# Kernel optimization log

Measured on AMD Instinct MI355X. Metric: run time of the kernel, lower is better.

Reference implementation:

```python
import jax, jax.numpy as jnp
import numpy as np

N = 100000
E = 3200000
D_IN = 83
D_HID = 1024
N_CLASSES = 25


def setup_inputs() -> dict:
    key = jax.random.key(0)
    ks = jax.random.split(key, 10)
    feature = jax.random.normal(ks[0], (N, D_IN), dtype=jnp.float32)
    edge_row = jax.random.randint(ks[1], (E,), 0, N, dtype=jnp.int32)
    edge_col = jax.random.randint(ks[2], (E,), 0, N, dtype=jnp.int32)
    adj_val = jax.random.uniform(ks[3], (E,), dtype=jnp.float32)
    # Conv1d(1 -> 4, kernel 5, pad 2): weight [out=4, in=1, k=5]
    conv_w = jax.random.normal(ks[4], (4, 1, 5), dtype=jnp.float32) * 0.2
    conv_b = jnp.zeros((4,), dtype=jnp.float32)
    # GCN weights (kaiming-uniform-like scale), zero biases
    W1 = jax.random.uniform(ks[5], (D_IN, D_HID), dtype=jnp.float32,
                            minval=-1.0, maxval=1.0) * np.sqrt(6.0 / D_IN)
    b1 = jnp.zeros((D_HID,), dtype=jnp.float32)
    W2 = jax.random.uniform(ks[6], (D_HID, N_CLASSES), dtype=jnp.float32,
                            minval=-1.0, maxval=1.0) * np.sqrt(6.0 / D_HID)
    b2 = jnp.zeros((N_CLASSES,), dtype=jnp.float32)
    return {"feature": feature, "conv_w": conv_w, "conv_b": conv_b,
            "W1": W1, "b1": b1, "W2": W2, "b2": b2,
            "adj_val": adj_val, "edge_row": edge_row, "edge_col": edge_col}


def _spmm(vals, row, col, X):
    # sparse(adj) @ X : gather source rows, scale by edge value, scatter-add to dest
    return jax.ops.segment_sum(vals[:, None] * X[col], row, num_segments=N)


def reference(feature, conv_w, conv_b, W1, b1, W2, b2, adj_val, edge_row, edge_col):
    # Conv1d prelude: [N,1,83] -> [N,4,83], sum over channels, relu -> [N,83]
    x = jax.lax.conv_general_dilated(
        feature[:, None, :], conv_w, window_strides=(1,), padding=[(2, 2)],
        dimension_numbers=("NCH", "OIH", "NCH"))
    x = x + conv_b[None, :, None]
    x = jax.nn.relu(jnp.sum(x, axis=1))
    # GCN layer 1: relu(A @ (x W1) + b1)
    h = jax.nn.relu(_spmm(adj_val, edge_row, edge_col, x @ W1) + b1)
    # GCN layer 2: A @ (h W2) + b2
    logits = _spmm(adj_val, edge_row, edge_col, h @ W2) + b2
    return logits
```

## Files before the change

kernel.cpp:

```cpp
#include <hip/hip_runtime.h>

#define NN   100000
#define EE   3200000
#define DIN  83
#define DHID 1024
#define NCLS 25
#define XPAD 96
#define ZPAD 32

#define NBK     391
#define CHUNK   8192

typedef __attribute__((__ext_vector_type__(8))) short sh8;
typedef __attribute__((__ext_vector_type__(4))) float f4_t;

static __device__ __forceinline__ float relu_(float v) { return v > 0.f ? v : 0.f; }

static __device__ __forceinline__ unsigned short f2bf(float f) {
  unsigned int u = __float_as_uint(f);
  unsigned int r = u + 0x7FFFu + ((u >> 16) & 1u);
  return (unsigned short)(r >> 16);
}
static __device__ __forceinline__ float bflo(unsigned int q) {
  return __uint_as_float(q << 16);
}
static __device__ __forceinline__ float bfhi(unsigned int q) {
  return __uint_as_float(q & 0xFFFF0000u);
}

__global__ void conv_relu_k(const float* __restrict__ feature,
                            const float* __restrict__ conv_w,
                            const float* __restrict__ conv_b,
                            unsigned short* __restrict__ x) {
  float ws0 = conv_w[0] + conv_w[5] + conv_w[10] + conv_w[15];
  float ws1 = conv_w[1] + conv_w[6] + conv_w[11] + conv_w[16];
  float ws2 = conv_w[2] + conv_w[7] + conv_w[12] + conv_w[17];
  float ws3 = conv_w[3] + conv_w[8] + conv_w[13] + conv_w[18];
  float ws4 = conv_w[4] + conv_w[9] + conv_w[14] + conv_w[19];
  float bs  = conv_b[0] + conv_b[1] + conv_b[2] + conv_b[3];
  const int total = NN * XPAD;
  for (int idx = blockIdx.x * blockDim.x + threadIdx.x; idx < total;
       idx += gridDim.x * blockDim.x) {
    int n = idx / XPAD;
    int i = idx - n * XPAD;
    unsigned short o = 0;
    if (i < DIN) {
      const float* f = feature + (size_t)n * DIN;
      float acc = bs;
      if (i >= 2)      acc += ws0 * f[i - 2];
      if (i >= 1)      acc += ws1 * f[i - 1];
      acc += ws2 * f[i];
      if (i + 1 < DIN) acc += ws3 * f[i + 1];
      if (i + 2 < DIN) acc += ws4 * f[i + 2];
      o = f2bf(relu_(acc));
    }
    x[idx] = o;
  }
}

__global__ void zero_int_k(int* __restrict__ p, int total) {
  for (int i = blockIdx.x * blockDim.x + threadIdx.x; i < total;
       i += gridDim.x * blockDim.x)
    p[i] = 0;
}

__global__ void w1t_k(const float* __restrict__ W1, unsigned short* __restrict__ w1t) {
  int idx = blockIdx.x * blockDim.x + threadIdx.x;
  if (idx >= DHID * XPAD) return;
  int k = idx / DHID;
  int n = idx - k * DHID;
  float v = (k < DIN) ? W1[k * DHID + n] : 0.f;
  w1t[n * XPAD + k] = f2bf(v);
}

__global__ void w2t_k(const float* __restrict__ W2, unsigned short* __restrict__ w2t) {
  int idx = blockIdx.x * blockDim.x + threadIdx.x;
  if (idx >= 32 * DHID) return;
  int k = idx / 32;
  int n = idx - k * 32;
  float v = (n < NCLS) ? W2[k * NCLS + n] : 0.f;
  w2t[n * DHID + k] = f2bf(v);
}


__global__ __launch_bounds__(256) void bucket_hist_k(
    const int* __restrict__ row, int* __restrict__ gbk) {
  __shared__ int cnt[NBK];
  const int tid = threadIdx.x;
  for (int b = tid; b < NBK; b += 256) cnt[b] = 0;
  __syncthreads();
  const int cb = blockIdx.x * CHUNK;
  const int csize = (cb + CHUNK <= EE) ? CHUNK : (EE - cb);
  for (int i = tid; i < csize; i += 256)
    atomicAdd(&cnt[row[cb + i] >> 8], 1);
  __syncthreads();
  for (int b = tid; b < NBK; b += 256)
    if (cnt[b]) atomicAdd(&gbk[b * 16], cnt[b]);
}

__global__ void scan_buckets_k(const int* __restrict__ gbk,
                               int* __restrict__ bbase, int* __restrict__ gcur) {
  __shared__ int sd[512];
  int t = threadIdx.x;
  int v = (t < NBK) ? gbk[t * 16] : 0;
  sd[t] = v;
  __syncthreads();
  for (int off = 1; off < 512; off <<= 1) {
    int add = (t >= off) ? sd[t - off] : 0;
    __syncthreads();
    sd[t] += add;
    __syncthreads();
  }
  if (t < NBK) {
    int excl = sd[t] - v;
    bbase[t] = excl;
    gcur[t * 16] = excl;
  }
  if (t == 0) bbase[NBK] = EE;
}

__global__ __launch_bounds__(256) void partition_k(
    const float* __restrict__ vals, const int* __restrict__ row,
    const int* __restrict__ col, int* __restrict__ gcur,
    int2* __restrict__ tmp) {
  __shared__ int cnt[NBK];
  __shared__ int sc[512];
  __shared__ int es[NBK + 1];
  __shared__ int lcur[NBK];
  __shared__ int gbase[NBK];
  __shared__ int2 staged[CHUNK];
  const int tid = threadIdx.x;
  const int cb = blockIdx.x * CHUNK;
  const int csize = (cb + CHUNK <= EE) ? CHUNK : (EE - cb);

  for (int b = tid; b < NBK; b += 256) cnt[b] = 0;
  __syncthreads();
  for (int i = tid; i < csize; i += 256)
    atomicAdd(&cnt[row[cb + i] >> 8], 1);
  __syncthreads();
  sc[tid]       = (tid < NBK) ? cnt[tid] : 0;
  sc[tid + 256] = (tid + 256 < NBK) ? cnt[tid + 256] : 0;
  __syncthreads();
  for (int off = 1; off < 512; off <<= 1) {
    int a0 = (tid >= off) ? sc[tid - off] : 0;
    int a1 = (tid + 256 >= off) ? sc[tid + 256 - off] : 0;
    __syncthreads();
    sc[tid] += a0;
    sc[tid + 256] += a1;
    __syncthreads();
  }
  for (int b = tid; b < NBK; b += 256) {
    int e = sc[b] - cnt[b];
    es[b] = e;
    lcur[b] = e;
  }
  if (tid == 0) es[NBK] = csize;
  __syncthreads();
  for (int b = tid; b < NBK; b += 256)
    gbase[b] = cnt[b] ? atomicAdd(&gcur[b * 16], cnt[b]) : 0;
  __syncthreads();
  for (int i = tid; i < csize; i += 256) {
    int r = row[cb + i];
    int lpos = atomicAdd(&lcur[r >> 8], 1);
    staged[lpos] = make_int2(col[cb + i] | ((r & 255) << 17),
                             __float_as_int(vals[cb + i]));
  }
  __syncthreads();
  {
    const int w = tid >> 6;
    const int lane = tid & 63;
    for (int b = w; b < NBK; b += 4) {
      int st = es[b], en = es[b + 1];
      int gb = gbase[b];
      for (int j = st + lane; j < en; j += 64)
        tmp[gb + (j - st)] = staged[j];
    }
  }
}

__global__ __launch_bounds__(256) void fine_scatter2_k(
    const int* __restrict__ bbase, const int2* __restrict__ tmp,
    int2* __restrict__ csr, int* __restrict__ offs, int* __restrict__ counts) {
  __shared__ int cnt[256];
  __shared__ int sd[256];
  __shared__ int lcur[256];
  const int tid = threadIdx.x;
  const int b = blockIdx.x;
  const int r0 = b * 256;
  const int gstart = bbase[b];
  const int nedge = bbase[b + 1] - gstart;
  cnt[tid] = 0;
  __syncthreads();
  for (int i = tid; i < nedge; i += 256)
    atomicAdd(&cnt[((unsigned)tmp[gstart + i].x) >> 17], 1);
  __syncthreads();
  int v = cnt[tid];
  sd[tid] = v;
  __syncthreads();
  for (int off = 1; off < 256; off <<= 1) {
    int add = (tid >= off) ? sd[tid - off] : 0;
    __syncthreads();
    sd[tid] += add;
    __syncthreads();
  }
  int excl = gstart + sd[tid] - v;
  int r = r0 + tid;
  if (r < NN) {
    offs[r] = excl;
    counts[r] = v;
  }
  lcur[tid] = excl;
  __syncthreads();
  for (int i = tid; i < nedge; i += 256) {
    int2 p = tmp[gstart + i];
    int rl = ((unsigned)p.x) >> 17;
    int pos = atomicAdd(&lcur[rl], 1);
    csr[pos] = make_int2(p.x & 0x1FFFF, p.y);
  }
}

__global__ __launch_bounds__(256) void spmm83_g(
    const int* __restrict__ offs, const int* __restrict__ cnt,
    const int2* __restrict__ csr, const unsigned short* __restrict__ x,
    unsigned short* __restrict__ ax) {
  int wave = (int)((blockIdx.x * blockDim.x + threadIdx.x) >> 6);
  int lane = threadIdx.x & 63;
  if (wave >= NN) return;
  int s = offs[wave];
  int n = cnt[wave];
  const bool act = lane < 48;
  const int d2 = lane * 2;
  float a0 = 0.f, a1 = 0.f;
  int i = 0;
  for (; i + 8 <= n; i += 8) {
    int2 p[8];
#pragma unroll
    for (int u = 0; u < 8; ++u) p[u] = csr[s + i + u];
    if (act) {
      unsigned int q[8];
#pragma unroll
      for (int u = 0; u < 8; ++u)
        q[u] = *(const unsigned int*)&x[(size_t)p[u].x * XPAD + d2];
#pragma unroll
      for (int u = 0; u < 8; ++u) {
        float v = __int_as_float(p[u].y);
        a0 += v * bflo(q[u]);
        a1 += v * bfhi(q[u]);
      }
    }
  }
  for (; i < n; ++i) {
    int2 p = csr[s + i];
    if (act) {
      unsigned int q = *(const unsigned int*)&x[(size_t)p.x * XPAD + d2];
      float v = __int_as_float(p.y);
      a0 += v * bflo(q);
      a1 += v * bfhi(q);
    }
  }
  if (act) {
    unsigned int o = (unsigned int)f2bf(a0) | ((unsigned int)f2bf(a1) << 16);
    *(unsigned int*)&ax[(size_t)wave * XPAD + d2] = o;
  }
}

__global__ __launch_bounds__(256) void spmm25_g(
    const int* __restrict__ offs, const int* __restrict__ cnt,
    const int2* __restrict__ csr, const unsigned short* __restrict__ zb,
    const float* __restrict__ b2, float* __restrict__ out) {
  int gw = (int)((blockIdx.x * blockDim.x + threadIdx.x) >> 6);
  int lane = threadIdx.x & 63;
  int sub = lane >> 4;
  int d2 = (lane & 15) * 2;
  int r = gw * 4 + sub;
  if (r >= NN) return;
  int s = offs[r];
  int n = cnt[r];
  float a0 = 0.f, a1 = 0.f;
  int i = 0;
  for (; i + 4 <= n; i += 4) {
    int2 p0 = csr[s + i + 0];
    int2 p1 = csr[s + i + 1];
    int2 p2 = csr[s + i + 2];
    int2 p3 = csr[s + i + 3];
    unsigned int q0 = *(const unsigned int*)&zb[(size_t)p0.x * ZPAD + d2];
    unsigned int q1 = *(const unsigned int*)&zb[(size_t)p1.x * ZPAD + d2];
    unsigned int q2 = *(const unsigned int*)&zb[(size_t)p2.x * ZPAD + d2];
    unsigned int q3 = *(const unsigned int*)&zb[(size_t)p3.x * ZPAD + d2];
    float v0 = __int_as_float(p0.y), v1 = __int_as_float(p1.y);
    float v2 = __int_as_float(p2.y), v3 = __int_as_float(p3.y);
    a0 += v0 * bflo(q0) + v1 * bflo(q1) + v2 * bflo(q2) + v3 * bflo(q3);
    a1 += v0 * bfhi(q0) + v1 * bfhi(q1) + v2 * bfhi(q2) + v3 * bfhi(q3);
  }
  for (; i < n; ++i) {
    int2 p = csr[s + i];
    unsigned int q = *(const unsigned int*)&zb[(size_t)p.x * ZPAD + d2];
    float v = __int_as_float(p.y);
    a0 += v * bflo(q);
    a1 += v * bfhi(q);
  }
  if (d2 < NCLS)     out[(size_t)r * NCLS + d2]     = a0 + b2[d2];
  if (d2 + 1 < NCLS) out[(size_t)r * NCLS + d2 + 1] = a1 + b2[d2 + 1];
}

__global__ __launch_bounds__(256) void fused_mlp_mfma(
    const unsigned short* __restrict__ axg, const unsigned short* __restrict__ w1t,
    const float* __restrict__ b1, const unsigned short* __restrict__ w2t,
    unsigned short* __restrict__ zb) {
  __shared__ __align__(16) unsigned short axs[64 * 104];
  __shared__ __align__(16) unsigned short hs[64 * 264];
  __shared__ float b1s[DHID];
  const int tid = threadIdx.x;
  const int n0 = blockIdx.x * 64;

  for (int idx = tid; idx < 64 * 12; idx += 256) {
    int m = idx / 12;
    int c8 = idx - m * 12;
    int node = n0 + m;
    sh8 v = {0, 0, 0, 0, 0, 0, 0, 0};
    if (node < NN) v = *(const sh8*)&axg[(size_t)node * XPAD + c8 * 8];
    *(sh8*)&axs[m * 104 + c8 * 8] = v;
  }
  for (int i = tid; i < DHID; i += 256) b1s[i] = b1[i];
  __syncthreads();

  const int lane = tid & 63;
  const int w = tid >> 6;
  const int quad = lane >> 4;
  const int tn = lane & 15;
  const int m0 = w * 16;

  sh8 a1[4][3];
#pragma unroll
  for (int mt = 0; mt < 4; ++mt)
#pragma unroll
    for (int kc = 0; kc < 3; ++kc)
      a1[mt][kc] = *(const sh8*)&axs[(mt * 16 + tn) * 104 + kc * 32 + quad * 8];

  f4_t z0 = {0.f, 0.f, 0.f, 0.f}, z1 = {0.f, 0.f, 0.f, 0.f};

  for (int c = 0; c < 4; ++c) {
    const int cb = c * 256;
#pragma unroll
    for (int nti = 0; nti < 4; ++nti) {
      const int nt = w * 4 + nti;
      const int ng = cb + nt * 16 + tn;
      const unsigned short* wr = &w1t[(size_t)ng * XPAD + quad * 8];
      sh8 b0 = *(const sh8*)&wr[0];
      sh8 b1f = *(const sh8*)&wr[32];
      sh8 b2f = *(const sh8*)&wr[64];
      float bias = b1s[ng];
#pragma unroll
      for (int mt = 0; mt < 4; ++mt) {
        f4_t acc = {0.f, 0.f, 0.f, 0.f};
        acc = __builtin_amdgcn_mfma_f32_16x16x32_bf16(a1[mt][0], b0, acc, 0, 0, 0);
        acc = __builtin_amdgcn_mfma_f32_16x16x32_bf16(a1[mt][1], b1f, acc, 0, 0, 0);
        acc = __builtin_amdgcn_mfma_f32_16x16x32_bf16(a1[mt][2], b2f, acc, 0, 0, 0);
#pragma unroll
        for (int r = 0; r < 4; ++r) {
          float v = relu_(acc[r] + bias);
          hs[(mt * 16 + quad * 4 + r) * 264 + nt * 16 + tn] = f2bf(v);
        }
      }
    }
    __syncthreads();
#pragma unroll
    for (int kc = 0; kc < 8; ++kc) {
      sh8 a2 = *(const sh8*)&hs[(m0 + tn) * 264 + kc * 32 + quad * 8];
      sh8 bl = *(const sh8*)&w2t[(size_t)tn * DHID + cb + kc * 32 + quad * 8];
      z0 = __builtin_amdgcn_mfma_f32_16x16x32_bf16(a2, bl, z0, 0, 0, 0);
      sh8 bh = *(const sh8*)&w2t[(size_t)(16 + tn) * DHID + cb + kc * 32 + quad * 8];
      z1 = __builtin_amdgcn_mfma_f32_16x16x32_bf16(a2, bh, z1, 0, 0, 0);
    }
    __syncthreads();
  }

#pragma unroll
  for (int r = 0; r < 4; ++r) {
    int node = n0 + m0 + quad * 4 + r;
    if (node < NN) {
      zb[(size_t)node * ZPAD + tn]      = f2bf(z0[r]);
      zb[(size_t)node * ZPAD + 16 + tn] = f2bf(z1[r]);
    }
  }
}

extern "C" void kernel_launch(void* const* d_in, const int* in_sizes, int n_in,
                              void* d_out, int out_size, void* d_ws, size_t ws_size,
                              hipStream_t stream) {
  const float* feature = (const float*)d_in[0];
  const float* conv_w  = (const float*)d_in[1];
  const float* conv_b  = (const float*)d_in[2];
  const float* W1      = (const float*)d_in[3];
  const float* b1      = (const float*)d_in[4];
  const float* W2      = (const float*)d_in[5];
  const float* b2      = (const float*)d_in[6];
  const float* adj     = (const float*)d_in[7];
  const int*   erow    = (const int*)d_in[8];
  const int*   ecol    = (const int*)d_in[9];
  float* out = (float*)d_out;

  char* B = (char*)d_ws;
  size_t o = 0;
  auto alloc = [&](size_t bytes, size_t align) -> void* {
    o = (o + align - 1) & ~(align - 1);
    void* p = B + o;
    o += bytes;
    return p;
  };
  unsigned short* x    = (unsigned short*)alloc((size_t)NN * XPAD * 2, 16);
  unsigned short* ax   = (unsigned short*)alloc((size_t)NN * XPAD * 2, 16);
  unsigned short* zb   = (unsigned short*)alloc((size_t)NN * ZPAD * 2, 16);
  int*   counts  = (int*)alloc((size_t)NN * 4, 16);
  int*   offs    = (int*)alloc((size_t)NN * 4, 16);
  int*   gcur    = (int*)alloc((size_t)NBK * 16 * 4, 64);
  int*   gbk     = (int*)alloc((size_t)NBK * 16 * 4, 64);
  int*   bbase   = (int*)alloc((size_t)(NBK + 1) * 4, 16);
  unsigned short* w1t = (unsigned short*)alloc((size_t)DHID * XPAD * 2, 16);
  unsigned short* w2t = (unsigned short*)alloc((size_t)32 * DHID * 2, 16);
  int2*  tmp     = (int2*)alloc((size_t)EE * 8, 16);
  int2*  csr     = (int2*)alloc((size_t)EE * 8, 16);

  conv_relu_k<<<8192, 256, 0, stream>>>(feature, conv_w, conv_b, x);
  w1t_k<<<(DHID * XPAD + 255) / 256, 256, 0, stream>>>(W1, w1t);
  w2t_k<<<(32 * DHID + 255) / 256, 256, 0, stream>>>(W2, w2t);
  zero_int_k<<<32, 256, 0, stream>>>(gbk, NBK * 16);
  bucket_hist_k<<<(EE + CHUNK - 1) / CHUNK, 256, 0, stream>>>(erow, gbk);
  scan_buckets_k<<<1, 512, 0, stream>>>(gbk, bbase, gcur);
  partition_k<<<(EE + CHUNK - 1) / CHUNK, 256, 0, stream>>>(adj, erow, ecol, gcur, tmp);
  fine_scatter2_k<<<NBK, 256, 0, stream>>>(bbase, tmp, csr, offs, counts);
  spmm83_g<<<(NN + 3) / 4, 256, 0, stream>>>(offs, counts, csr, x, ax);
  fused_mlp_mfma<<<(NN + 63) / 64, 256, 0, stream>>>(ax, w1t, b1, w2t, zb);
  spmm25_g<<<(NN + 15) / 16, 256, 0, stream>>>(offs, counts, csr, zb, b2, out);
}
```

Before: 504.1 us.

## Widen fused MLP tile to 128 nodes, merge prep kernels, scalarize spmm offsets

The fused MLP kernel now handles 128 nodes per block in 128-wide hidden chunks instead of 64 nodes in 256-wide chunks. Each W1 and W2 fragment loaded from global memory is therefore reused across twice as many rows. The weight transposes and bucket-counter zeroing are merged into one prep kernel to cut launches. In spmm83, the row offset and count go through readfirstlane so they are held in scalar registers. The trade-off is more VGPR pressure from a1[8][3] and the doubled chunk loop, which may reduce occupancy, and half as many MLP blocks.

```diff
diff --git a/kernel.cpp b/kernel.cpp
--- a/kernel.cpp
+++ b/kernel.cpp
@@ -58,28 +58,23 @@
   }
 }
 
-__global__ void zero_int_k(int* __restrict__ p, int total) {
-  for (int i = blockIdx.x * blockDim.x + threadIdx.x; i < total;
-       i += gridDim.x * blockDim.x)
-    p[i] = 0;
-}
-
-__global__ void w1t_k(const float* __restrict__ W1, unsigned short* __restrict__ w1t) {
+__global__ void prep_k(const float* __restrict__ W1, unsigned short* __restrict__ w1t,
+                       const float* __restrict__ W2, unsigned short* __restrict__ w2t,
+                       int* __restrict__ gbk) {
   int idx = blockIdx.x * blockDim.x + threadIdx.x;
-  if (idx >= DHID * XPAD) return;
-  int k = idx / DHID;
-  int n = idx - k * DHID;
-  float v = (k < DIN) ? W1[k * DHID + n] : 0.f;
-  w1t[n * XPAD + k] = f2bf(v);
-}
-
-__global__ void w2t_k(const float* __restrict__ W2, unsigned short* __restrict__ w2t) {
-  int idx = blockIdx.x * blockDim.x + threadIdx.x;
-  if (idx >= 32 * DHID) return;
-  int k = idx / 32;
-  int n = idx - k * 32;
-  float v = (n < NCLS) ? W2[k * NCLS + n] : 0.f;
-  w2t[n * DHID + k] = f2bf(v);
+  if (idx < DHID * XPAD) {
+    int k = idx / DHID;
+    int n = idx - k * DHID;
+    float v = (k < DIN) ? W1[k * DHID + n] : 0.f;
+    w1t[n * XPAD + k] = f2bf(v);
+  }
+  if (idx < 32 * DHID) {
+    int k = idx / 32;
+    int n = idx - k * 32;
+    float v = (n < NCLS) ? W2[k * NCLS + n] : 0.f;
+    w2t[n * DHID + k] = f2bf(v);
+  }
+  if (idx < NBK * 16) gbk[idx] = 0;
 }
 
 
@@ -226,8 +221,8 @@
   int wave = (int)((blockIdx.x * blockDim.x + threadIdx.x) >> 6);
   int lane = threadIdx.x & 63;
   if (wave >= NN) return;
-  int s = offs[wave];
-  int n = cnt[wave];
+  int s = __builtin_amdgcn_readfirstlane(offs[wave]);
+  int n = __builtin_amdgcn_readfirstlane(cnt[wave]);
   const bool act = lane < 48;
   const int d2 = lane * 2;
   float a0 = 0.f, a1 = 0.f;
@@ -307,13 +302,13 @@
     const unsigned short* __restrict__ axg, const unsigned short* __restrict__ w1t,
     const float* __restrict__ b1, const unsigned short* __restrict__ w2t,
     unsigned short* __restrict__ zb) {
-  __shared__ __align__(16) unsigned short axs[64 * 104];
-  __shared__ __align__(16) unsigned short hs[64 * 264];
+  __shared__ __align__(16) unsigned short axs[128 * 104];
+  __shared__ __align__(16) unsigned short hs[128 * 136];
   __shared__ float b1s[DHID];
   const int tid = threadIdx.x;
-  const int n0 = blockIdx.x * 64;
-
-  for (int idx = tid; idx < 64 * 12; idx += 256) {
+  const int n0 = blockIdx.x * 128;
+
+  for (int idx = tid; idx < 128 * 12; idx += 256) {
     int m = idx / 12;
     int c8 = idx - m * 12;
     int node = n0 + m;
@@ -328,22 +323,24 @@
   const int w = tid >> 6;
   const int quad = lane >> 4;
   const int tn = lane & 15;
-  const int m0 = w * 16;
-
-  sh8 a1[4][3];
-#pragma unroll
-  for (int mt = 0; mt < 4; ++mt)
+  const int mta = w;
+  const int mtb = w + 4;
+
+  sh8 a1[8][3];
+#pragma unroll
+  for (int mt = 0; mt < 8; ++mt)
 #pragma unroll
     for (int kc = 0; kc < 3; ++kc)
       a1[mt][kc] = *(const sh8*)&axs[(mt * 16 + tn) * 104 + kc * 32 + quad * 8];
 
-  f4_t z0 = {0.f, 0.f, 0.f, 0.f}, z1 = {0.f, 0.f, 0.f, 0.f};
-
-  for (int c = 0; c < 4; ++c) {
-    const int cb = c * 256;
-#pragma unroll
-    for (int nti = 0; nti < 4; ++nti) {
-      const int nt = w * 4 + nti;
+  f4_t za0 = {0.f, 0.f, 0.f, 0.f}, za1 = {0.f, 0.f, 0.f, 0.f};
+  f4_t zb0 = {0.f, 0.f, 0.f, 0.f}, zb1 = {0.f, 0.f, 0.f, 0.f};
+
+  for (int c = 0; c < 8; ++c) {
+    const int cb = c * 128;
+#pragma unroll
+    for (int nti = 0; nti < 2; ++nti) {
+      const int nt = w * 2 + nti;
       const int ng = cb + nt * 16 + tn;
       const unsigned short* wr = &w1t[(size_t)ng * XPAD + quad * 8];
       sh8 b0 = *(const sh8*)&wr[0];
@@ -351,7 +348,7 @@
       sh8 b2f = *(const sh8*)&wr[64];
       float bias = b1s[ng];
 #pragma unroll
-      for (int mt = 0; mt < 4; ++mt) {
+      for (int mt = 0; mt < 8; ++mt) {
         f4_t acc = {0.f, 0.f, 0.f, 0.f};
         acc = __builtin_amdgcn_mfma_f32_16x16x32_bf16(a1[mt][0], b0, acc, 0, 0, 0);
         acc = __builtin_amdgcn_mfma_f32_16x16x32_bf16(a1[mt][1], b1f, acc, 0, 0, 0);
@@ -359,28 +356,36 @@
 #pragma unroll
         for (int r = 0; r < 4; ++r) {
           float v = relu_(acc[r] + bias);
-          hs[(mt * 16 + quad * 4 + r) * 264 + nt * 16 + tn] = f2bf(v);
+          hs[(mt * 16 + quad * 4 + r) * 136 + nt * 16 + tn] = f2bf(v);
         }
       }
     }
     __syncthreads();
 #pragma unroll
-    for (int kc = 0; kc < 8; ++kc) {
-      sh8 a2 = *(const sh8*)&hs[(m0 + tn) * 264 + kc * 32 + quad * 8];
+    for (int kc = 0; kc < 4; ++kc) {
       sh8 bl = *(const sh8*)&w2t[(size_t)tn * DHID + cb + kc * 32 + quad * 8];
-      z0 = __builtin_amdgcn_mfma_f32_16x16x32_bf16(a2, bl, z0, 0, 0, 0);
       sh8 bh = *(const sh8*)&w2t[(size_t)(16 + tn) * DHID + cb + kc * 32 + quad * 8];
-      z1 = __builtin_amdgcn_mfma_f32_16x16x32_bf16(a2, bh, z1, 0, 0, 0);
+      sh8 aa = *(const sh8*)&hs[(mta * 16 + tn) * 136 + kc * 32 + quad * 8];
+      za0 = __builtin_amdgcn_mfma_f32_16x16x32_bf16(aa, bl, za0, 0, 0, 0);
+      za1 = __builtin_amdgcn_mfma_f32_16x16x32_bf16(aa, bh, za1, 0, 0, 0);
+      sh8 ab = *(const sh8*)&hs[(mtb * 16 + tn) * 136 + kc * 32 + quad * 8];
+      zb0 = __builtin_amdgcn_mfma_f32_16x16x32_bf16(ab, bl, zb0, 0, 0, 0);
+      zb1 = __builtin_amdgcn_mfma_f32_16x16x32_bf16(ab, bh, zb1, 0, 0, 0);
     }
     __syncthreads();
   }
 
 #pragma unroll
   for (int r = 0; r < 4; ++r) {
-    int node = n0 + m0 + quad * 4 + r;
-    if (node < NN) {
-      zb[(size_t)node * ZPAD + tn]      = f2bf(z0[r]);
-      zb[(size_t)node * ZPAD + 16 + tn] = f2bf(z1[r]);
+    int na = n0 + mta * 16 + quad * 4 + r;
+    if (na < NN) {
+      zb[(size_t)na * ZPAD + tn]      = f2bf(za0[r]);
+      zb[(size_t)na * ZPAD + 16 + tn] = f2bf(za1[r]);
+    }
+    int nb = n0 + mtb * 16 + quad * 4 + r;
+    if (nb < NN) {
+      zb[(size_t)nb * ZPAD + tn]      = f2bf(zb0[r]);
+      zb[(size_t)nb * ZPAD + 16 + tn] = f2bf(zb1[r]);
     }
   }
 }
@@ -422,14 +427,12 @@
   int2*  csr     = (int2*)alloc((size_t)EE * 8, 16);
 
   conv_relu_k<<<8192, 256, 0, stream>>>(feature, conv_w, conv_b, x);
-  w1t_k<<<(DHID * XPAD + 255) / 256, 256, 0, stream>>>(W1, w1t);
-  w2t_k<<<(32 * DHID + 255) / 256, 256, 0, stream>>>(W2, w2t);
-  zero_int_k<<<32, 256, 0, stream>>>(gbk, NBK * 16);
+  prep_k<<<(DHID * XPAD + 255) / 256, 256, 0, stream>>>(W1, w1t, W2, w2t, gbk);
   bucket_hist_k<<<(EE + CHUNK - 1) / CHUNK, 256, 0, stream>>>(erow, gbk);
   scan_buckets_k<<<1, 512, 0, stream>>>(gbk, bbase, gcur);
   partition_k<<<(EE + CHUNK - 1) / CHUNK, 256, 0, stream>>>(adj, erow, ecol, gcur, tmp);
   fine_scatter2_k<<<NBK, 256, 0, stream>>>(bbase, tmp, csr, offs, counts);
   spmm83_g<<<(NN + 3) / 4, 256, 0, stream>>>(offs, counts, csr, x, ax);
-  fused_mlp_mfma<<<(NN + 63) / 64, 256, 0, stream>>>(ax, w1t, b1, w2t, zb);
+  fused_mlp_mfma<<<(NN + 127) / 128, 256, 0, stream>>>(ax, w1t, b1, w2t, zb);
   spmm25_g<<<(NN + 15) / 16, 256, 0, stream>>>(offs, counts, csr, zb, b2, out);
 }
```

Measured after the change: 479.0 us. 1.05x faster.
